# Performance work log

Measured on AMD Instinct MI355X. Metric: run time of the kernel, lower is better.

Reference implementation:

```python
import jax, jax.numpy as jnp
import numpy as np

INV_L_MIN, INV_L_MAX = 0.5, 2.0

def _gelu(v):
    return jax.nn.gelu(v, approximate=False)  # torch F.gelu default = exact erf

def compute_gradient(f, directed_edges, edge_gradient_weights):
    # f: [b, c, n] ; directed_edges: [b, e, 2] (target, source) ; egw: [b, e, d]
    f = jnp.transpose(f, (0, 2, 1))                      # [b, n, c]
    b, n, c = f.shape
    e, d = edge_gradient_weights.shape[1], edge_gradient_weights.shape[2]
    target, source = directed_edges[..., 0], directed_edges[..., 1]
    fs = jnp.take_along_axis(f, source[:, :, None], axis=1)   # [b, e, c]
    ft = jnp.take_along_axis(f, target[:, :, None], axis=1)   # [b, e, c]
    # einsum('bed,bec->becd') then reshape -> channel-major (c*d) layout
    msg = (edge_gradient_weights[:, :, None, :] * (fs - ft)[:, :, :, None]).reshape(b, e, c * d)
    seg = (target + n * jnp.arange(b, dtype=target.dtype)[:, None]).reshape(-1)
    grad = jax.ops.segment_sum(msg.reshape(b * e, c * d), seg, num_segments=b * n)
    return jnp.transpose(grad.reshape(b, n, c * d), (0, 2, 1))  # [b, c*d, n]

def spectral_conv(x, wc, ws_, w0, bc, bs, b0, wbc, wbs, wb0):
    # x: [b, c, n]; bases: [b, n, k, w]; weights: [c, o, k, w]
    xc = jnp.einsum('bcx,bxkw->bckw', x, wbc)
    xs = jnp.einsum('bcx,bxkw->bckw', x, wbs)
    x0 = jnp.einsum('bcx,bxkw->bckw', x, wb0)
    fc = jnp.einsum('bckw,cokw->bokw', xc, wc) - jnp.einsum('bckw,cokw->bokw', xs, ws_)
    fs = jnp.einsum('bckw,cokw->bokw', xs, wc) + jnp.einsum('bckw,cokw->bokw', xc, ws_)
    f0 = jnp.einsum('bckw,cokw->bokw', x0, w0)
    return (jnp.einsum('bokw,bxkw->box', f0, b0)
            + 2 * jnp.einsum('bokw,bxkw->box', fc, bc)
            - 2 * jnp.einsum('bokw,bxkw->box', fs, bs))

def setup_inputs():
    key = jax.random.key(0)
    ks = jax.random.split(key, 16)
    B, N, E = 4, 20000, 100000
    NDIMS, NMEAS, NMODES = 3, 1, 32
    C, L = 128, 3
    IN_DIM, FC_DIM, OUT_DIM = 3, 128, 1
    f32 = jnp.float32
    inp = {}
    inp['x'] = jax.random.normal(ks[0], (B, N, IN_DIM), f32)
    inp['node_mask'] = jnp.ones((B, N, 1), jnp.int32)
    inp['nodes'] = jax.random.uniform(ks[1], (B, N, NDIMS), f32)
    inp['node_weights'] = jax.random.uniform(ks[2], (B, N, NMEAS), f32) / N
    inp['directed_edges'] = jax.random.randint(ks[3], (B, E, 2), 0, N, jnp.int32)
    inp['edge_gradient_weights'] = jax.random.normal(ks[4], (B, E, NDIMS), f32)
    # modes k = 2*pi*K/L0, K integer-like
    inp['modes'] = (2 * jnp.pi * jax.random.randint(ks[5], (NMODES, NDIMS, NMEAS), 1, 9)).astype(f32)
    # scaled_logit(1.0, 0.5, 2.0): sigmoid(l)=1/3 -> l=log(0.5)
    inp['inv_L_scale_latent'] = jnp.full((NDIMS, NMEAS), np.log(0.5), f32)
    inp['fc0_w'] = jax.random.normal(ks[6], (C, IN_DIM), f32) / np.sqrt(IN_DIM)
    inp['fc0_b'] = jnp.zeros((C,), f32)
    sc = 1.0 / (C * C)
    inp['swc'] = sc * jax.random.uniform(ks[7], (L, C, C, NMODES, NMEAS), f32)
    inp['sws'] = sc * jax.random.uniform(ks[8], (L, C, C, NMODES, NMEAS), f32)
    inp['sw0'] = sc * jax.random.uniform(ks[9], (L, C, C, 1, NMEAS), f32)
    inp['ww'] = jax.random.normal(ks[10], (L, C, C), f32) / np.sqrt(C)
    inp['wb'] = jnp.zeros((L, C), f32)
    inp['gw'] = jax.random.normal(ks[11], (L, C, NDIMS * C), f32) / np.sqrt(NDIMS * C)
    inp['gb'] = jnp.zeros((L, C), f32)
    inp['fc1_w'] = jax.random.normal(ks[12], (FC_DIM, C), f32) / np.sqrt(C)
    inp['fc1_b'] = jnp.zeros((FC_DIM,), f32)
    inp['fc2_w'] = jax.random.normal(ks[13], (OUT_DIM, FC_DIM), f32) / np.sqrt(FC_DIM)
    inp['fc2_b'] = jnp.zeros((OUT_DIM,), f32)
    return inp

def reference(x, node_mask, nodes, node_weights, directed_edges, edge_gradient_weights,
              modes, inv_L_scale_latent, fc0_w, fc0_b, swc, sws, sw0, ww, wb, gw, gb,
              fc1_w, fc1_b, fc2_w, fc2_b):
    inv_L = INV_L_MIN + (INV_L_MAX - INV_L_MIN) * jax.nn.sigmoid(inv_L_scale_latent)  # [d, w]
    t = jnp.einsum('bxd,kdw->bxkw', nodes, modes * inv_L[None])
    bc, bs = jnp.cos(t), jnp.sin(t)
    b0 = jnp.ones(t.shape[:2] + (1, t.shape[3]), t.dtype)
    w = node_weights[:, :, None, :]
    wbc, wbs, wb0 = bc * w, bs * w, b0 * w
    h = jnp.einsum('bni,ci->bnc', x, fc0_w) + fc0_b        # lift
    h = jnp.transpose(h, (0, 2, 1))                        # [b, C, n]
    L = swc.shape[0]
    for i in range(L):
        h1 = spectral_conv(h, swc[i], sws[i], sw0[i], bc, bs, b0, wbc, wbs, wb0)
        h2 = jnp.einsum('oc,bcn->bon', ww[i], h) + wb[i][None, :, None]
        g = compute_gradient(h, directed_edges, edge_gradient_weights)
        h3 = jnp.einsum('oc,bcn->bon', gw[i], g) + gb[i][None, :, None]
        h = h1 + h2 + h3
        if i != L - 1:
            h = _gelu(h)
    h = jnp.transpose(h, (0, 2, 1))                        # [b, n, C]
    h = _gelu(h @ fc1_w.T + fc1_b)
    return h @ fc2_w.T + fc2_b                             # [b, n, out_dim]
```

## Files before the change

### kernel.cpp

```cpp
#include <hip/hip_runtime.h>
#include <math.h>

#define B_ 4
#define N_ 20000
#define E_ 100000
#define C_ 128
#define K_ 32
#define NPAD 20480
#define NROWS (B_*N_ + 128)

typedef __attribute__((ext_vector_type(8))) short short8;
typedef __attribute__((ext_vector_type(4))) float floatx4;
typedef __attribute__((ext_vector_type(4))) unsigned int uintx4;
typedef __attribute__((ext_vector_type(2))) unsigned int uintx2;

__device__ __forceinline__ float gelu_exact(float x){
    return 0.5f * x * (1.0f + erff(x * 0.70710678118654752f));
}

__device__ __forceinline__ unsigned short f2bf(float f){
    unsigned int u = __builtin_bit_cast(unsigned int, f);
    u += 0x7FFFu + ((u >> 16) & 1u);
    return (unsigned short)(u >> 16);
}
__device__ __forceinline__ unsigned int pack2(float a, float b){
    return (unsigned int)f2bf(a) | ((unsigned int)f2bf(b) << 16);
}
__device__ __forceinline__ float bf2f(unsigned short u){
    unsigned int v = ((unsigned int)u) << 16;
    return __builtin_bit_cast(float, v);
}
__device__ __forceinline__ float u2f(unsigned int u){
    return __builtin_bit_cast(float, u);
}


__global__ __launch_bounds__(256) void basis_kernel(
    const float* __restrict__ nodes, const float* __restrict__ nw,
    const float* __restrict__ modes, const float* __restrict__ latent,
    unsigned short* __restrict__ bcb, unsigned short* __restrict__ bsb,
    unsigned short* __restrict__ wBt)
{
    __shared__ float lx[64], ly[64], lz[64], lwv[64];
    __shared__ unsigned short lTc[32*64], lTs[32*64];
    int b = blockIdx.y, n0 = blockIdx.x*64;
    int tid = threadIdx.x;
    size_t bN = (size_t)b*N_;
    if (tid < 64){
        int n = n0 + tid;
        float iL0 = 0.5f + 1.5f/(1.f+expf(-latent[0]));
        float iL1 = 0.5f + 1.5f/(1.f+expf(-latent[1]));
        float iL2 = 0.5f + 1.5f/(1.f+expf(-latent[2]));
        if (n < N_){
            lx[tid] = nodes[(bN+n)*3+0]*iL0;
            ly[tid] = nodes[(bN+n)*3+1]*iL1;
            lz[tid] = nodes[(bN+n)*3+2]*iL2;
            lwv[tid] = nw[bN+n];
        } else { lx[tid]=0.f; ly[tid]=0.f; lz[tid]=0.f; lwv[tid]=0.f; }
    }
    __syncthreads();
    int node = tid>>2, k0 = (tid&3)*8;
    float p0 = lx[node], p1 = ly[node], p2 = lz[node], w = lwv[node];
    float cv[8], sv[8];
    #pragma unroll
    for (int i=0;i<8;i++){
        int k = k0+i;
        float t = p0*modes[k*3+0] + p1*modes[k*3+1] + p2*modes[k*3+2];
        cv[i] = cosf(t); sv[i] = sinf(t);
        lTc[k*64 + node] = f2bf(w*cv[i]);
        lTs[k*64 + node] = f2bf(w*sv[i]);
    }
    int gn = n0 + node;
    if (gn < N_){
        uintx4 uc = (uintx4){pack2(cv[0],cv[1]), pack2(cv[2],cv[3]),
                             pack2(cv[4],cv[5]), pack2(cv[6],cv[7])};
        uintx4 us = (uintx4){pack2(sv[0],sv[1]), pack2(sv[2],sv[3]),
                             pack2(sv[4],sv[5]), pack2(sv[6],sv[7])};
        *(uintx4*)&bcb[(bN+gn)*K_ + k0] = uc;
        *(uintx4*)&bsb[(bN+gn)*K_ + k0] = us;
    }
    __syncthreads();
    #pragma unroll
    for (int i=0;i<5;i++){
        int idx = i*256 + tid;
        int row = idx>>4, seg = idx&15;
        unsigned short v0,v1,v2,v3;
        if (row < 32){
            v0=lTc[row*64+seg*4+0]; v1=lTc[row*64+seg*4+1];
            v2=lTc[row*64+seg*4+2]; v3=lTc[row*64+seg*4+3];
        } else if (row < 64){
            int r = row-32;
            v0=lTs[r*64+seg*4+0]; v1=lTs[r*64+seg*4+1];
            v2=lTs[r*64+seg*4+2]; v3=lTs[r*64+seg*4+3];
        } else if (row == 64){
            v0=f2bf(lwv[seg*4+0]); v1=f2bf(lwv[seg*4+1]);
            v2=f2bf(lwv[seg*4+2]); v3=f2bf(lwv[seg*4+3]);
        } else { v0=v1=v2=v3=0; }
        uintx2 u;
        u.x = (unsigned int)v0 | ((unsigned int)v1<<16);
        u.y = (unsigned int)v2 | ((unsigned int)v3<<16);
        *(uintx2*)&wBt[((size_t)b*80+row)*NPAD + n0 + seg*4] = u;
    }
}


__global__ __launch_bounds__(256) void fc0_kernel(
    const float* __restrict__ x, const float* __restrict__ w,
    const float* __restrict__ bvec, unsigned short* __restrict__ hN,
    unsigned short* __restrict__ hT)
{
    int idx = blockIdx.x*256 + threadIdx.x;
    if (idx >= B_*N_) return;
    int b = idx / N_, n = idx - b*N_;
    float x0 = x[(size_t)idx*3+0], x1 = x[(size_t)idx*3+1], x2 = x[(size_t)idx*3+2];
    unsigned short* hr = hN + (size_t)idx*C_;
    for (int c=0;c<C_;c+=4){
        float4 v;
        v.x = bvec[c+0] + x0*w[(c+0)*3] + x1*w[(c+0)*3+1] + x2*w[(c+0)*3+2];
        v.y = bvec[c+1] + x0*w[(c+1)*3] + x1*w[(c+1)*3+1] + x2*w[(c+1)*3+2];
        v.z = bvec[c+2] + x0*w[(c+2)*3] + x1*w[(c+2)*3+1] + x2*w[(c+2)*3+2];
        v.w = bvec[c+3] + x0*w[(c+3)*3] + x1*w[(c+3)*3+1] + x2*w[(c+3)*3+2];
        uintx2 u; u.x = pack2(v.x,v.y); u.y = pack2(v.z,v.w);
        *(uintx2*)(hr+c) = u;
        hT[((size_t)b*C_+c+0)*NPAD + n] = f2bf(v.x);
        hT[((size_t)b*C_+c+1)*NPAD + n] = f2bf(v.y);
        hT[((size_t)b*C_+c+2)*NPAD + n] = f2bf(v.z);
        hT[((size_t)b*C_+c+3)*NPAD + n] = f2bf(v.w);
    }
}


__global__ __launch_bounds__(256) void hist_kernel(
    const int* __restrict__ edges, int* __restrict__ cnt)
{
    int idx = blockIdx.x*256 + threadIdx.x;
    if (idx >= B_*E_) return;
    int b = idx / E_;
    int t = edges[(size_t)idx*2];
    atomicAdd(cnt + b*N_ + t, 1);
}

__global__ __launch_bounds__(1024) void scan_kernel(
    const int* __restrict__ cnt, int* __restrict__ rowptr, int* __restrict__ cur)
{
    __shared__ int wsum[16];
    int b = blockIdx.x, tid = threadIdx.x;
    int lane = tid & 63, wv = tid >> 6;
    const int CHUNK = 20;
    int start = tid * CHUNK;
    int lc[CHUNK];
    int lsum = 0;
    #pragma unroll
    for (int i=0;i<CHUNK;i++){
        int n = start + i;
        int v = (n < N_) ? cnt[b*N_+n] : 0;
        lc[i] = v; lsum += v;
    }
    int v = lsum;
    #pragma unroll
    for (int off=1; off<64; off<<=1){
        int t = __shfl_up(v, off, 64);
        if (lane >= off) v += t;
    }
    if (lane == 63) wsum[wv] = v;
    __syncthreads();
    if (wv == 0 && lane < 16){
        int wv2 = wsum[lane];
        #pragma unroll
        for (int off=1; off<16; off<<=1){
            int t = __shfl_up(wv2, off, 64);
            if (lane >= off) wv2 += t;
        }
        wsum[lane] = wv2;
    }
    __syncthreads();
    int waveoff = (wv == 0) ? 0 : wsum[wv-1];
    int excl = waveoff + v - lsum;
    #pragma unroll
    for (int i=0;i<CHUNK;i++){
        int n = start + i;
        if (n < N_){
            rowptr[b*(N_+1)+n] = excl;
            cur[b*N_+n] = excl;
            excl += lc[i];
        }
    }
    if (tid == 0) rowptr[b*(N_+1)+N_] = E_;
}

__global__ __launch_bounds__(256) void fill_kernel(
    const int* __restrict__ edges, const float* __restrict__ egw,
    int* __restrict__ cur, uintx4* __restrict__ epack)
{
    int idx = blockIdx.x*256 + threadIdx.x;
    if (idx >= B_*E_) return;
    int b = idx / E_;
    int t = edges[(size_t)idx*2];
    int src = edges[(size_t)idx*2+1];
    uintx4 rec;
    rec.x = (unsigned int)src;
    rec.y = __builtin_bit_cast(unsigned int, egw[(size_t)idx*3+0]);
    rec.z = __builtin_bit_cast(unsigned int, egw[(size_t)idx*3+1]);
    rec.w = __builtin_bit_cast(unsigned int, egw[(size_t)idx*3+2]);
    int pos = atomicAdd(cur + b*N_ + t, 1);
    epack[(size_t)b*E_ + pos] = rec;
}


__global__ __launch_bounds__(256) void wconv_kernel(
    const float* __restrict__ ww, const float* __restrict__ gw,
    unsigned short* __restrict__ wcat3)
{
    int o = blockIdx.x, l = blockIdx.y, t = threadIdx.x;
    const float* ww_l = ww + (size_t)l*C_*C_;
    const float* gw_l = gw + (size_t)l*C_*C_*3;
    int k = t*2;
    float a, bv;
    if (k < 128){ a = ww_l[(size_t)o*C_ + k];      bv = ww_l[(size_t)o*C_ + k + 1]; }
    else        { a = gw_l[(size_t)o*384 + k-128]; bv = gw_l[(size_t)o*384 + k-127]; }
    *(unsigned int*)&wcat3[((size_t)l*C_ + o)*512 + k] = pack2(a, bv);
}

__global__ __launch_bounds__(64) void fc1conv_kernel(
    const float* __restrict__ fc1w, unsigned short* __restrict__ w16)
{
    int o = blockIdx.x, t = threadIdx.x;
    int k = t*2;
    *(unsigned int*)&w16[(size_t)o*C_ + k] = pack2(fc1w[(size_t)o*C_+k], fc1w[(size_t)o*C_+k+1]);
}


__global__ __launch_bounds__(256) void stageA_kernel(
    const unsigned short* __restrict__ hT, const unsigned short* __restrict__ wBt,
    float* __restrict__ part)
{
    __shared__ unsigned short As[80*72];
    __shared__ unsigned short Bs[128*72];
    int b = blockIdx.y, blk = blockIdx.x;
    int tid = threadIdx.x;
    int wv = tid>>6, lane = tid&63, l15 = lane&15, quad = lane>>4;
    floatx4 acc[5][2];
    #pragma unroll
    for (int mt=0;mt<5;mt++){ acc[mt][0]=(floatx4){0,0,0,0}; acc[mt][1]=(floatx4){0,0,0,0}; }
    size_t hbase = (size_t)b*C_*NPAD;
    size_t wbase = (size_t)b*80*NPAD;
    for (int cidx=0; cidx<5; ++cidx){
        int n0c = blk*320 + cidx*64;
        #pragma unroll
        for (int i=0;i<3;i++){
            int idx = i*256 + tid;
            if (idx < 640){
                int row = idx>>3, seg = idx&7;
                uintx4 v = *(const uintx4*)&wBt[wbase + (size_t)row*NPAD + n0c + seg*8];
                *(uintx4*)&As[row*72 + seg*8] = v;
            }
        }
        #pragma unroll
        for (int i=0;i<4;i++){
            int idx = i*256 + tid;
            int row = idx>>3, seg = idx&7;
            int node = n0c + seg*8;
            uintx4 v = (uintx4){0,0,0,0};
            if (node < N_)
                v = *(const uintx4*)&hT[hbase + (size_t)row*NPAD + node];
            *(uintx4*)&Bs[row*72 + seg*8] = v;
        }
        __syncthreads();
        #pragma unroll
        for (int ks=0; ks<2; ks++){
            short8 bfrag[2];
            #pragma unroll
            for (int ot=0;ot<2;ot++)
                bfrag[ot] = *(const short8*)&Bs[(wv*32+ot*16+l15)*72 + ks*32 + quad*8];
            #pragma unroll
            for (int mt=0;mt<5;mt++){
                short8 af = *(const short8*)&As[(mt*16+l15)*72 + ks*32 + quad*8];
                acc[mt][0] = __builtin_amdgcn_mfma_f32_16x16x32_bf16(af, bfrag[0], acc[mt][0], 0,0,0);
                acc[mt][1] = __builtin_amdgcn_mfma_f32_16x16x32_bf16(af, bfrag[1], acc[mt][1], 0,0,0);
            }
        }
        __syncthreads();
    }
    float* pblk = part + ((size_t)(b*64+blk))*80*C_;
    #pragma unroll
    for (int mt=0;mt<5;mt++){
        #pragma unroll
        for (int ot=0;ot<2;ot++){
            int c = wv*32 + ot*16 + l15;
            #pragma unroll
            for (int r=0;r<4;r++){
                int kcol = mt*16 + quad*4 + r;
                pblk[kcol*C_ + c] = acc[mt][ot][r];
            }
        }
    }
}

__global__ __launch_bounds__(256) void reducePart_kernel(
    const float* __restrict__ part, float* __restrict__ xq)
{
    int idx = blockIdx.x*256 + threadIdx.x;
    if (idx >= B_*80*C_) return;
    int b = idx / (80*C_);
    int r = idx - b*80*C_;
    float s = 0.f;
    for (int blk=0; blk<64; blk++)
        s += part[((size_t)(b*64+blk))*80*C_ + r];
    xq[idx] = s;
}


__global__ __launch_bounds__(256) void mix_kernel(
    const float* __restrict__ xq, const float* __restrict__ swc_l,
    const float* __restrict__ sws_l, const float* __restrict__ sw0_l,
    unsigned short* __restrict__ wfb, float* __restrict__ f0)
{
    __shared__ float s64[4][64];
    int o = blockIdx.x, tid = threadIdx.x;
    int b = tid >> 6, t = tid & 63;
    int k = t & 31; bool isS = t >= 32;
    const float* xqb = xq + (size_t)b*80*C_;
    float acc = 0.f;
    for (int c=0;c<C_;c++){
        float xc = xqb[k*C_ + c], xs = xqb[(32+k)*C_ + c];
        float wc = swc_l[((size_t)c*C_+o)*K_ + k];
        float ws = sws_l[((size_t)c*C_+o)*K_ + k];
        acc += isS ? (xs*wc + xc*ws) : (xc*wc - xs*ws);
    }
    wfb[((size_t)b*C_+o)*64 + t] = f2bf(isS ? -2.f*acc : 2.f*acc);
    float p = xqb[64*C_ + t]      * sw0_l[(size_t)t*C_+o]
            + xqb[64*C_ + 64 + t] * sw0_l[(size_t)(t+64)*C_+o];
    s64[b][t] = p; __syncthreads();
    if (t==0){
        float s=0.f;
        for (int i=0;i<64;i++) s += s64[b][i];
        f0[b*C_+o] = s;
    }
}


__global__ __launch_bounds__(256) void grad_kernel(
    const unsigned short* __restrict__ hN, const uintx4* __restrict__ epack,
    const int* __restrict__ rowptr, unsigned short* __restrict__ g)
{
    int flat = blockIdx.x;
    int xcd = flat & 7;
    int b = xcd >> 1;
    int grp = (flat >> 3)*2 + (xcd & 1);
    int n = grp*4 + (threadIdx.x >> 6);
    int cp = threadIdx.x & 63;
    size_t bN = (size_t)b*N_;
    size_t bE = (size_t)b*E_;
    int r0 = rowptr[b*(N_+1)+n], r1 = rowptr[b*(N_+1)+n+1];
    unsigned int hcu = *(const unsigned int*)&hN[(bN+n)*C_ + cp*2];
    float hc0 = bf2f((unsigned short)hcu), hc1 = bf2f((unsigned short)(hcu>>16));
    float a00=0.f,a01=0.f,a02=0.f, a10=0.f,a11=0.f,a12=0.f;
    int i = r0;
    for (; i + 1 < r1; i += 2){
        uintx4 p0 = epack[bE + i];
        uintx4 p1 = epack[bE + i + 1];
        int s0 = (int)p0.x, s1 = (int)p1.x;
        unsigned int u0 = *(const unsigned int*)&hN[(bN+s0)*C_ + cp*2];
        unsigned int u1 = *(const unsigned int*)&hN[(bN+s1)*C_ + cp*2];
        float w00 = u2f(p0.y), w01 = u2f(p0.z), w02 = u2f(p0.w);
        float w10 = u2f(p1.y), w11 = u2f(p1.z), w12 = u2f(p1.w);
        float d00 = bf2f((unsigned short)u0) - hc0;
        float d01 = bf2f((unsigned short)(u0>>16)) - hc1;
        float d10 = bf2f((unsigned short)u1) - hc0;
        float d11 = bf2f((unsigned short)(u1>>16)) - hc1;
        a00 += w00*d00; a01 += w01*d00; a02 += w02*d00;
        a10 += w00*d01; a11 += w01*d01; a12 += w02*d01;
        a00 += w10*d10; a01 += w11*d10; a02 += w12*d10;
        a10 += w10*d11; a11 += w11*d11; a12 += w12*d11;
    }
    if (i < r1){
        uintx4 p0 = epack[bE + i];
        int s0 = (int)p0.x;
        unsigned int u0 = *(const unsigned int*)&hN[(bN+s0)*C_ + cp*2];
        float w00 = u2f(p0.y), w01 = u2f(p0.z), w02 = u2f(p0.w);
        float d00 = bf2f((unsigned short)u0) - hc0;
        float d01 = bf2f((unsigned short)(u0>>16)) - hc1;
        a00 += w00*d00; a01 += w01*d00; a02 += w02*d00;
        a10 += w00*d01; a11 += w01*d01; a12 += w02*d01;
    }
    unsigned short* gr = g + (bN+n)*(size_t)384 + cp*6;
    *(unsigned int*)(gr+0) = pack2(a00,a01);
    *(unsigned int*)(gr+2) = pack2(a02,a10);
    *(unsigned int*)(gr+4) = pack2(a11,a12);
}


#define WAITV(n) asm volatile("s_waitcnt vmcnt(" #n ")" ::: "memory")
#define BAR() __builtin_amdgcn_s_barrier()

__global__ __launch_bounds__(256) void gemm_kernel(
    const unsigned short* __restrict__ hN, const unsigned short* __restrict__ g,
    const unsigned short* __restrict__ bcb, const unsigned short* __restrict__ bsb,
    const unsigned short* __restrict__ wcat, const unsigned short* __restrict__ wfb,
    const float* __restrict__ wb_l, const float* __restrict__ gb_l,
    const float* __restrict__ f0,
    unsigned short* __restrict__ hNo, unsigned short* __restrict__ hT, int apply_gelu)
{
    __shared__ unsigned short As4[4][4096];
    int b = blockIdx.y;
    int nb0 = blockIdx.x*64;
    int tid = threadIdx.x;
    int wv = tid>>6, lane = tid&63, l15 = lane&15, quad = lane>>4;
    floatx4 acc[4][2];
    #pragma unroll
    for (int mt=0;mt<4;mt++)
        #pragma unroll
        for (int ot=0;ot<2;ot++) acc[mt][ot] = (floatx4){0.f,0.f,0.f,0.f};
    size_t bN = (size_t)b*N_;

    const unsigned short* sh[2]; const unsigned short* sg[2]; const unsigned short* sb[2];
    #pragma unroll
    for (int q=0;q<2;q++){
        int li = q*256 + tid;
        int row = li>>3, col = (li&7) ^ (row&7);
        size_t gr = bN + (size_t)(nb0 + row);
        sh[q] = hN + gr*C_  + col*8;
        sg[q] = g  + gr*384 + col*8;
        sb[q] = (col < 4) ? (bcb + gr*K_ + col*8) : (bsb + gr*K_ + (col-4)*8);
    }
    int o0 = wv*32 + l15, o1 = o0 + 16;
    const unsigned short* w0p = wcat + (size_t)o0*512 + quad*8;
    const unsigned short* w1p = wcat + (size_t)o1*512 + quad*8;
    const unsigned short* fb0 = wfb + ((size_t)b*C_ + o0)*64 + quad*8;
    const unsigned short* fb1 = wfb + ((size_t)b*C_ + o1)*64 + quad*8;

    short8 bb[3][2][2];

#define LOADB(ch) do{ \
    if ((ch) < 8){ \
        bb[(ch)%3][0][0] = *(const short8*)(w0p + (ch)*64); \
        bb[(ch)%3][0][1] = *(const short8*)(w0p + (ch)*64 + 32); \
        bb[(ch)%3][1][0] = *(const short8*)(w1p + (ch)*64); \
        bb[(ch)%3][1][1] = *(const short8*)(w1p + (ch)*64 + 32); \
    } else { \
        bb[(ch)%3][0][0] = *(const short8*)(fb0); \
        bb[(ch)%3][0][1] = *(const short8*)(fb0 + 32); \
        bb[(ch)%3][1][0] = *(const short8*)(fb1); \
        bb[(ch)%3][1][1] = *(const short8*)(fb1 + 32); \
    } }while(0)

#define STAGE1(ch,q) \
    __builtin_amdgcn_global_load_lds( \
        (const __attribute__((address_space(1))) void*)( \
            ((ch) < 2) ? (sh[q] + (ch)*64) : \
            ((ch) < 8) ? (sg[q] + ((ch)-2)*64) : sb[q] ), \
        (__attribute__((address_space(3))) void*)&As4[(ch)&3][(q)*2048 + wv*512], \
        16, 0, 0)
#define STAGE(ch) do{ STAGE1(ch,0); STAGE1(ch,1); }while(0)

#define COMPUTE(ch) do{ \
    _Pragma("unroll") \
    for (int ks=0; ks<2; ks++){ \
        _Pragma("unroll") \
        for (int mt=0; mt<4; mt++){ \
            short8 af = *(const short8*)&As4[(ch)&3][(mt*16+l15)*64 + (((ks*4+quad)^(l15&7))*8)]; \
            acc[mt][0] = __builtin_amdgcn_mfma_f32_16x16x32_bf16(af, bb[(ch)%3][0][ks], acc[mt][0], 0,0,0); \
            acc[mt][1] = __builtin_amdgcn_mfma_f32_16x16x32_bf16(af, bb[(ch)%3][1][ks], acc[mt][1], 0,0,0); \
        } } }while(0)

    LOADB(0); LOADB(1);
    STAGE(0); STAGE(1); STAGE(2);
    WAITV(4); BAR(); LOADB(2); STAGE(3); COMPUTE(0);
    WAITV(8); BAR(); LOADB(3); STAGE(4); COMPUTE(1);
    WAITV(8); BAR(); LOADB(4); STAGE(5); COMPUTE(2);
    WAITV(8); BAR(); LOADB(5); STAGE(6); COMPUTE(3);
    WAITV(8); BAR(); LOADB(6); STAGE(7); COMPUTE(4);
    WAITV(8); BAR(); LOADB(7); STAGE(8); COMPUTE(5);
    WAITV(8); BAR(); LOADB(8);           COMPUTE(6);
    WAITV(6); BAR();                     COMPUTE(7);
    WAITV(0); BAR();                     COMPUTE(8);

#undef LOADB
#undef STAGE1
#undef STAGE
#undef COMPUTE

    float biasv[2]; int oo[2];
    oo[0]=o0; oo[1]=o1;
    #pragma unroll
    for (int ot=0;ot<2;ot++)
        biasv[ot] = wb_l[oo[ot]] + gb_l[oo[ot]] + f0[(size_t)b*C_ + oo[ot]];
    unsigned short* AsF = &As4[0][0];
    if (apply_gelu) __syncthreads();
    #pragma unroll
    for (int mt=0;mt<4;mt++){
        #pragma unroll
        for (int ot=0;ot<2;ot++){
            int nb = nb0 + mt*16 + quad*4;
            float v4[4];
            #pragma unroll
            for (int r=0;r<4;r++){
                float vv = acc[mt][ot][r] + biasv[ot];
                if (apply_gelu) vv = gelu_exact(vv);
                v4[r] = vv;
                if (nb + r < N_) hNo[(bN+nb+r)*C_ + oo[ot]] = f2bf(vv);
            }
            if (apply_gelu){
                uintx2 u; u.x = pack2(v4[0],v4[1]); u.y = pack2(v4[2],v4[3]);
                *(uintx2*)&AsF[oo[ot]*72 + mt*16 + quad*4] = u;
            }
        }
    }
    if (apply_gelu){
        __syncthreads();
        int orow = tid>>1, half = tid&1;
        uintx4 u0 = *(const uintx4*)&AsF[orow*72 + half*32];
        uintx4 u1 = *(const uintx4*)&AsF[orow*72 + half*32 + 8];
        unsigned short* dst = &hT[((size_t)b*C_ + orow)*NPAD + nb0 + half*32];
        *(uintx4*)dst       = u0;
        *(uintx4*)(dst + 8) = u1;
    }
}


__global__ __launch_bounds__(256) void final_kernel(
    const unsigned short* __restrict__ hN, const unsigned short* __restrict__ fc1b16,
    const float* __restrict__ fc1b, const float* __restrict__ fc2w,
    const float* __restrict__ fc2b, float* __restrict__ out)
{
    __shared__ unsigned short As[64*72];
    __shared__ float pp[4*64];
    int b = blockIdx.y;
    int nb0 = blockIdx.x*64;
    int tid = threadIdx.x;
    int a_n = tid>>2, a_s = tid&3;
    int wv = tid>>6, lane = tid&63, l15 = lane&15, quad = lane>>4;
    floatx4 acc[4][2];
    #pragma unroll
    for (int mt=0;mt<4;mt++){ acc[mt][0]=(floatx4){0,0,0,0}; acc[mt][1]=(floatx4){0,0,0,0}; }
    size_t bN = (size_t)b*N_;
    int gn = nb0 + a_n; bool av = gn < N_;
    size_t row = bN + (size_t)(av ? gn : 0);
    const unsigned short* hrow = hN + row*C_;
    int o0 = wv*32 + l15, o1 = o0 + 16;
    const unsigned short* w0p = fc1b16 + (size_t)o0*C_ + quad*8;
    const unsigned short* w1p = fc1b16 + (size_t)o1*C_ + quad*8;

    for (int ch=0; ch<2; ++ch){
        uintx4 v0 = (uintx4){0,0,0,0}, v1 = (uintx4){0,0,0,0};
        if (av){
            const uintx4* pptr = (const uintx4*)(hrow + ch*64 + a_s*16);
            v0 = pptr[0]; v1 = pptr[1];
        }
        *(uintx4*)&As[a_n*72 + a_s*16]     = v0;
        *(uintx4*)&As[a_n*72 + a_s*16 + 8] = v1;
        __syncthreads();
        #pragma unroll
        for (int ks=0; ks<2; ks++){
            short8 bfr0 = *(const short8*)(w0p + ch*64 + ks*32);
            short8 bfr1 = *(const short8*)(w1p + ch*64 + ks*32);
            #pragma unroll
            for (int mt=0; mt<4; mt++){
                short8 af = *(const short8*)&As[(mt*16+l15)*72 + ks*32 + quad*8];
                acc[mt][0] = __builtin_amdgcn_mfma_f32_16x16x32_bf16(af, bfr0, acc[mt][0], 0,0,0);
                acc[mt][1] = __builtin_amdgcn_mfma_f32_16x16x32_bf16(af, bfr1, acc[mt][1], 0,0,0);
            }
        }
        __syncthreads();
    }
    float fw0 = fc2w[o0], fw1 = fc2w[o1];
    float b0 = fc1b[o0], b1 = fc1b[o1];
    #pragma unroll
    for (int mt=0;mt<4;mt++){
        float s[4];
        #pragma unroll
        for (int r=0;r<4;r++)
            s[r] = fw0*gelu_exact(acc[mt][0][r] + b0) + fw1*gelu_exact(acc[mt][1][r] + b1);
        #pragma unroll
        for (int m=1;m<16;m<<=1)
            #pragma unroll
            for (int r=0;r<4;r++)
                s[r] += __shfl_xor(s[r], m, 16);
        if (l15 < 4){
            float v = (l15==0)?s[0]:(l15==1)?s[1]:(l15==2)?s[2]:s[3];
            pp[wv*64 + mt*16 + quad*4 + l15] = v;
        }
    }
    __syncthreads();
    if (tid < 64){
        float sum = pp[tid] + pp[64+tid] + pp[128+tid] + pp[192+tid] + fc2b[0];
        int n = nb0 + tid;
        if (n < N_) out[bN + n] = sum;
    }
}


extern "C" void kernel_launch(void* const* d_in, const int* in_sizes, int n_in,
                              void* d_out, int out_size, void* d_ws, size_t ws_size,
                              hipStream_t stream)
{
    const float* x      = (const float*)d_in[0];
    const float* nodes  = (const float*)d_in[2];
    const float* nw     = (const float*)d_in[3];
    const int*   edges  = (const int*)  d_in[4];
    const float* egw    = (const float*)d_in[5];
    const float* modes  = (const float*)d_in[6];
    const float* latent = (const float*)d_in[7];
    const float* fc0w   = (const float*)d_in[8];
    const float* fc0b   = (const float*)d_in[9];
    const float* swc    = (const float*)d_in[10];
    const float* sws    = (const float*)d_in[11];
    const float* sw0    = (const float*)d_in[12];
    const float* ww     = (const float*)d_in[13];
    const float* wb     = (const float*)d_in[14];
    const float* gw     = (const float*)d_in[15];
    const float* gb     = (const float*)d_in[16];
    const float* fc1w   = (const float*)d_in[17];
    const float* fc1b   = (const float*)d_in[18];
    const float* fc2w   = (const float*)d_in[19];
    const float* fc2b   = (const float*)d_in[20];
    float* out = (float*)d_out;

    char* W = (char*)d_ws;
    size_t off = 0;
    unsigned short* bcB = (unsigned short*)(W+off); off += (size_t)NROWS*K_*2;
    unsigned short* bsB = (unsigned short*)(W+off); off += (size_t)NROWS*K_*2;
    unsigned short* wBt = (unsigned short*)(W+off); off += (size_t)B_*80*NPAD*2;
    unsigned short* hT  = (unsigned short*)(W+off); off += (size_t)B_*C_*NPAD*2;
    unsigned short* hNa = (unsigned short*)(W+off); off += (size_t)NROWS*C_*2;
    unsigned short* hNb = (unsigned short*)(W+off); off += (size_t)NROWS*C_*2;
    unsigned short* g   = (unsigned short*)(W+off); off += (size_t)NROWS*C_*3*2;
    unsigned short* wcat3=(unsigned short*)(W+off); off += (size_t)3*C_*512*2;
    unsigned short* wfb = (unsigned short*)(W+off); off += (size_t)B_*C_*64*2;
    unsigned short* fcw16=(unsigned short*)(W+off); off += (size_t)C_*C_*2;
    float* part = (float*)(W+off); off += (size_t)B_*64*80*C_*4;
    float* xq   = (float*)(W+off); off += (size_t)B_*80*C_*4;
    float* f0   = (float*)(W+off); off += (size_t)B_*C_*4;
    off = (off + 15) & ~(size_t)15;
    uintx4* epack = (uintx4*)(W+off); off += (size_t)B_*E_*16;
    int* cnt    = (int*)(W+off); off += (size_t)B_*N_*4;
    int* rowptr = (int*)(W+off); off += (size_t)B_*(N_+1)*4 + 16;
    int* cur    = (int*)(W+off); off += (size_t)B_*N_*4;

    (void)hipMemsetAsync(cnt, 0, (size_t)B_*N_*sizeof(int), stream);
    basis_kernel<<<dim3(NPAD/64, B_), 256, 0, stream>>>(
        nodes, nw, modes, latent, bcB, bsB, wBt);
    fc0_kernel  <<<(B_*N_+255)/256, 256, 0, stream>>>(x, fc0w, fc0b, hNa, hT);
    hist_kernel <<<(B_*E_+255)/256, 256, 0, stream>>>(edges, cnt);
    scan_kernel <<<B_, 1024, 0, stream>>>(cnt, rowptr, cur);
    fill_kernel <<<(B_*E_+255)/256, 256, 0, stream>>>(edges, egw, cur, epack);
    wconv_kernel<<<dim3(C_,3), 256, 0, stream>>>(ww, gw, wcat3);
    fc1conv_kernel<<<C_, 64, 0, stream>>>(fc1w, fcw16);

    unsigned short* hc = hNa; unsigned short* hn = hNb;
    for (int l=0; l<3; ++l){
        stageA_kernel<<<dim3(64,B_), 256, 0, stream>>>(hT, wBt, part);
        reducePart_kernel<<<(B_*80*C_+255)/256, 256, 0, stream>>>(part, xq);
        mix_kernel<<<C_, 256, 0, stream>>>(
            xq, swc + (size_t)l*C_*C_*K_, sws + (size_t)l*C_*C_*K_,
            sw0 + (size_t)l*C_*C_, wfb, f0);
        grad_kernel<<<N_, 256, 0, stream>>>(hc, epack, rowptr, g);
        gemm_kernel<<<dim3((N_+63)/64,B_), 256, 0, stream>>>(
            hc, g, bcB, bsB, wcat3 + (size_t)l*C_*512, wfb,
            wb + (size_t)l*C_, gb + (size_t)l*C_,
            f0, hn, hT, (l<2) ? 1 : 0);
        unsigned short* t = hc; hc = hn; hn = t;
    }
    final_kernel<<<dim3((N_+63)/64,B_), 256, 0, stream>>>(
        hc, fcw16, fc1b, fc2w, fc2b, out);
}
```

Before: 548.6 us.

## Double-buffer stageA with direct global-to-LDS loads and unroll gradient gather by four

stageA now stages both operand tiles into a double-buffered, XOR-swizzled LDS array using global_load_lds. The next chunk's loads overlap the current chunk's MFMAs, replacing the earlier load-sync-compute loop. To make unguarded loads safe, fc0 and the gemm epilogue now zero the padded hT columns beyond N. The grad kernel's edge loop is unrolled from two to four edges so more gathers are in flight, at the cost of more registers.

```diff
diff --git a/kernel.cpp b/kernel.cpp
--- a/kernel.cpp
+++ b/kernel.cpp
@@ -33,6 +33,9 @@
 __device__ __forceinline__ float u2f(unsigned int u){
     return __builtin_bit_cast(float, u);
 }
+
+#define WAITV(n) asm volatile("s_waitcnt vmcnt(" #n ")" ::: "memory")
+#define BAR() __builtin_amdgcn_s_barrier()
 
 
 __global__ __launch_bounds__(256) void basis_kernel(
@@ -110,10 +113,16 @@
     unsigned short* __restrict__ hT)
 {
     int idx = blockIdx.x*256 + threadIdx.x;
-    if (idx >= B_*N_) return;
-    int b = idx / N_, n = idx - b*N_;
-    float x0 = x[(size_t)idx*3+0], x1 = x[(size_t)idx*3+1], x2 = x[(size_t)idx*3+2];
-    unsigned short* hr = hN + (size_t)idx*C_;
+    if (idx >= B_*NPAD) return;
+    int b = idx / NPAD, n = idx - b*NPAD;
+    if (n >= N_){
+        for (int c=0;c<C_;c++)
+            hT[((size_t)b*C_+c)*NPAD + n] = 0;
+        return;
+    }
+    size_t idn = (size_t)b*N_ + n;
+    float x0 = x[idn*3+0], x1 = x[idn*3+1], x2 = x[idn*3+2];
+    unsigned short* hr = hN + idn*C_;
     for (int c=0;c<C_;c+=4){
         float4 v;
         v.x = bvec[c+0] + x0*w[(c+0)*3] + x1*w[(c+0)*3+1] + x2*w[(c+0)*3+2];
@@ -234,8 +243,7 @@
     const unsigned short* __restrict__ hT, const unsigned short* __restrict__ wBt,
     float* __restrict__ part)
 {
-    __shared__ unsigned short As[80*72];
-    __shared__ unsigned short Bs[128*72];
+    __shared__ unsigned short stg[2][224*64];
     int b = blockIdx.y, blk = blockIdx.x;
     int tid = threadIdx.x;
     int wv = tid>>6, lane = tid&63, l15 = lane&15, quad = lane>>4;
@@ -244,43 +252,49 @@
     for (int mt=0;mt<5;mt++){ acc[mt][0]=(floatx4){0,0,0,0}; acc[mt][1]=(floatx4){0,0,0,0}; }
     size_t hbase = (size_t)b*C_*NPAD;
     size_t wbase = (size_t)b*80*NPAD;
-    for (int cidx=0; cidx<5; ++cidx){
-        int n0c = blk*320 + cidx*64;
-        #pragma unroll
-        for (int i=0;i<3;i++){
-            int idx = i*256 + tid;
-            if (idx < 640){
-                int row = idx>>3, seg = idx&7;
-                uintx4 v = *(const uintx4*)&wBt[wbase + (size_t)row*NPAD + n0c + seg*8];
-                *(uintx4*)&As[row*72 + seg*8] = v;
-            }
-        }
-        #pragma unroll
-        for (int i=0;i<4;i++){
-            int idx = i*256 + tid;
-            int row = idx>>3, seg = idx&7;
-            int node = n0c + seg*8;
-            uintx4 v = (uintx4){0,0,0,0};
-            if (node < N_)
-                v = *(const uintx4*)&hT[hbase + (size_t)row*NPAD + node];
-            *(uintx4*)&Bs[row*72 + seg*8] = v;
-        }
-        __syncthreads();
-        #pragma unroll
-        for (int ks=0; ks<2; ks++){
-            short8 bfrag[2];
-            #pragma unroll
-            for (int ot=0;ot<2;ot++)
-                bfrag[ot] = *(const short8*)&Bs[(wv*32+ot*16+l15)*72 + ks*32 + quad*8];
-            #pragma unroll
-            for (int mt=0;mt<5;mt++){
-                short8 af = *(const short8*)&As[(mt*16+l15)*72 + ks*32 + quad*8];
-                acc[mt][0] = __builtin_amdgcn_mfma_f32_16x16x32_bf16(af, bfrag[0], acc[mt][0], 0,0,0);
-                acc[mt][1] = __builtin_amdgcn_mfma_f32_16x16x32_bf16(af, bfrag[1], acc[mt][1], 0,0,0);
-            }
-        }
-        __syncthreads();
-    }
+    int n0 = blk*320;
+    const unsigned short* sp[7];
+    #pragma unroll
+    for (int q=0;q<7;q++){
+        int li = q*256 + tid;
+        int r = li>>3;
+        int u = (li&7) ^ (r&7);
+        int rw = (r < 80) ? r : 79;
+        sp[q] = (r < 96) ? (wBt + wbase + (size_t)rw*NPAD + n0 + u*8)
+                         : (hT  + hbase + (size_t)(r-96)*NPAD + n0 + u*8);
+    }
+
+#define SSTG(ch) do{ \
+    _Pragma("unroll") \
+    for (int q=0;q<7;q++) \
+        __builtin_amdgcn_global_load_lds( \
+            (const __attribute__((address_space(1))) void*)(sp[q] + (ch)*64), \
+            (__attribute__((address_space(3))) void*)&stg[(ch)&1][q*2048 + wv*512], \
+            16, 0, 0); }while(0)
+
+#define SCOMP(ch) do{ \
+    _Pragma("unroll") \
+    for (int ks=0; ks<2; ks++){ \
+        short8 bfrag[2]; \
+        _Pragma("unroll") \
+        for (int ot=0;ot<2;ot++) \
+            bfrag[ot] = *(const short8*)&stg[(ch)&1][(96 + wv*32 + ot*16 + l15)*64 + (((ks*4+quad)^(l15&7))*8)]; \
+        _Pragma("unroll") \
+        for (int mt=0;mt<5;mt++){ \
+            short8 af = *(const short8*)&stg[(ch)&1][(mt*16+l15)*64 + (((ks*4+quad)^(l15&7))*8)]; \
+            acc[mt][0] = __builtin_amdgcn_mfma_f32_16x16x32_bf16(af, bfrag[0], acc[mt][0], 0,0,0); \
+            acc[mt][1] = __builtin_amdgcn_mfma_f32_16x16x32_bf16(af, bfrag[1], acc[mt][1], 0,0,0); \
+        } } }while(0)
+
+    SSTG(0); SSTG(1);
+    WAITV(7); BAR(); SCOMP(0); BAR(); SSTG(2);
+    WAITV(7); BAR(); SCOMP(1); BAR(); SSTG(3);
+    WAITV(7); BAR(); SCOMP(2); BAR(); SSTG(4);
+    WAITV(7); BAR(); SCOMP(3);
+    WAITV(0); BAR(); SCOMP(4);
+#undef SSTG
+#undef SCOMP
+
     float* pblk = part + ((size_t)(b*64+blk))*80*C_;
     #pragma unroll
     for (int mt=0;mt<5;mt++){
@@ -356,27 +370,31 @@
     float hc0 = bf2f((unsigned short)hcu), hc1 = bf2f((unsigned short)(hcu>>16));
     float a00=0.f,a01=0.f,a02=0.f, a10=0.f,a11=0.f,a12=0.f;
     int i = r0;
-    for (; i + 1 < r1; i += 2){
+    for (; i + 3 < r1; i += 4){
         uintx4 p0 = epack[bE + i];
         uintx4 p1 = epack[bE + i + 1];
-        int s0 = (int)p0.x, s1 = (int)p1.x;
-        unsigned int u0 = *(const unsigned int*)&hN[(bN+s0)*C_ + cp*2];
-        unsigned int u1 = *(const unsigned int*)&hN[(bN+s1)*C_ + cp*2];
-        float w00 = u2f(p0.y), w01 = u2f(p0.z), w02 = u2f(p0.w);
-        float w10 = u2f(p1.y), w11 = u2f(p1.z), w12 = u2f(p1.w);
-        float d00 = bf2f((unsigned short)u0) - hc0;
-        float d01 = bf2f((unsigned short)(u0>>16)) - hc1;
-        float d10 = bf2f((unsigned short)u1) - hc0;
-        float d11 = bf2f((unsigned short)(u1>>16)) - hc1;
-        a00 += w00*d00; a01 += w01*d00; a02 += w02*d00;
-        a10 += w00*d01; a11 += w01*d01; a12 += w02*d01;
-        a00 += w10*d10; a01 += w11*d10; a02 += w12*d10;
-        a10 += w10*d11; a11 += w11*d11; a12 += w12*d11;
-    }
-    if (i < r1){
+        uintx4 p2 = epack[bE + i + 2];
+        uintx4 p3 = epack[bE + i + 3];
+        unsigned int u0 = *(const unsigned int*)&hN[(bN+(int)p0.x)*C_ + cp*2];
+        unsigned int u1 = *(const unsigned int*)&hN[(bN+(int)p1.x)*C_ + cp*2];
+        unsigned int u2 = *(const unsigned int*)&hN[(bN+(int)p2.x)*C_ + cp*2];
+        unsigned int u3 = *(const unsigned int*)&hN[(bN+(int)p3.x)*C_ + cp*2];
+        float d00 = bf2f((unsigned short)u0) - hc0, d01 = bf2f((unsigned short)(u0>>16)) - hc1;
+        float d10 = bf2f((unsigned short)u1) - hc0, d11 = bf2f((unsigned short)(u1>>16)) - hc1;
+        float d20 = bf2f((unsigned short)u2) - hc0, d21 = bf2f((unsigned short)(u2>>16)) - hc1;
+        float d30 = bf2f((unsigned short)u3) - hc0, d31 = bf2f((unsigned short)(u3>>16)) - hc1;
+        a00 += u2f(p0.y)*d00; a01 += u2f(p0.z)*d00; a02 += u2f(p0.w)*d00;
+        a10 += u2f(p0.y)*d01; a11 += u2f(p0.z)*d01; a12 += u2f(p0.w)*d01;
+        a00 += u2f(p1.y)*d10; a01 += u2f(p1.z)*d10; a02 += u2f(p1.w)*d10;
+        a10 += u2f(p1.y)*d11; a11 += u2f(p1.z)*d11; a12 += u2f(p1.w)*d11;
+        a00 += u2f(p2.y)*d20; a01 += u2f(p2.z)*d20; a02 += u2f(p2.w)*d20;
+        a10 += u2f(p2.y)*d21; a11 += u2f(p2.z)*d21; a12 += u2f(p2.w)*d21;
+        a00 += u2f(p3.y)*d30; a01 += u2f(p3.z)*d30; a02 += u2f(p3.w)*d30;
+        a10 += u2f(p3.y)*d31; a11 += u2f(p3.z)*d31; a12 += u2f(p3.w)*d31;
+    }
+    for (; i < r1; ++i){
         uintx4 p0 = epack[bE + i];
-        int s0 = (int)p0.x;
-        unsigned int u0 = *(const unsigned int*)&hN[(bN+s0)*C_ + cp*2];
+        unsigned int u0 = *(const unsigned int*)&hN[(bN+(int)p0.x)*C_ + cp*2];
         float w00 = u2f(p0.y), w01 = u2f(p0.z), w02 = u2f(p0.w);
         float d00 = bf2f((unsigned short)u0) - hc0;
         float d01 = bf2f((unsigned short)(u0>>16)) - hc1;
@@ -389,9 +407,6 @@
     *(unsigned int*)(gr+4) = pack2(a11,a12);
 }
 
-
-#define WAITV(n) asm volatile("s_waitcnt vmcnt(" #n ")" ::: "memory")
-#define BAR() __builtin_amdgcn_s_barrier()
 
 __global__ __launch_bounds__(256) void gemm_kernel(
     const unsigned short* __restrict__ hN, const unsigned short* __restrict__ g,
@@ -497,8 +512,9 @@
             for (int r=0;r<4;r++){
                 float vv = acc[mt][ot][r] + biasv[ot];
                 if (apply_gelu) vv = gelu_exact(vv);
-                v4[r] = vv;
-                if (nb + r < N_) hNo[(bN+nb+r)*C_ + oo[ot]] = f2bf(vv);
+                bool ok = (nb + r < N_);
+                if (ok) hNo[(bN+nb+r)*C_ + oo[ot]] = f2bf(vv);
+                v4[r] = ok ? vv : 0.f;
             }
             if (apply_gelu){
                 uintx2 u; u.x = pack2(v4[0],v4[1]); u.y = pack2(v4[2],v4[3]);
@@ -640,7 +656,7 @@
     (void)hipMemsetAsync(cnt, 0, (size_t)B_*N_*sizeof(int), stream);
     basis_kernel<<<dim3(NPAD/64, B_), 256, 0, stream>>>(
         nodes, nw, modes, latent, bcB, bsB, wBt);
-    fc0_kernel  <<<(B_*N_+255)/256, 256, 0, stream>>>(x, fc0w, fc0b, hNa, hT);
+    fc0_kernel  <<<(B_*NPAD+255)/256, 256, 0, stream>>>(x, fc0w, fc0b, hNa, hT);
     hist_kernel <<<(B_*E_+255)/256, 256, 0, stream>>>(edges, cnt);
     scan_kernel <<<B_, 1024, 0, stream>>>(cnt, rowptr, cur);
     fill_kernel <<<(B_*E_+255)/256, 256, 0, stream>>>(edges, egw, cur, epack);
```

Measured after the change: 527.6 us. 1.04x faster.
